# Optimization experiments

Hardware: AMD Instinct MI355X
Metric: run time of the kernel (lower is better)

Reference implementation:

```python
import jax, jax.numpy as jnp
import numpy as np

WINDOWS = [7, 15, 31, 63, 127]
MAX_W = max(WINDOWS)
PAD = MAX_W // 2 + 1  # 64, matches K.spatial_2d_padding amount
HALF = MAX_W // 2     # 63


def _sat(a):
    """Integral image (summed-area table) of zero-padded input, per original layer."""
    ap = jnp.pad(a, ((0, 0), (PAD, PAD), (PAD, PAD), (0, 0)))
    return jnp.cumsum(jnp.cumsum(ap, axis=1), axis=2)


def _multi_window_means(a):
    """Box means for all window sizes. a: [B,H,W,C] -> [B,n_wins,H,W,C].
    Computes the count SAT once (original redundantly recomputes it per window;
    math is identical)."""
    B, H, W, C = a.shape
    ii = _sat(a)
    cnt_ii = _sat(jnp.ones_like(a[:1, ..., :1]))  # [1, H+2P, W+2P, 1]

    def box(ii_, h, w):
        top = HALF - h // 2
        left = HALF - w // 2
        bot, right = top + h, left + w
        return (ii_[:, top:top + H, left:left + W]
                + ii_[:, bot:bot + H, right:right + W]
                - ii_[:, top:top + H, right:right + W]
                - ii_[:, bot:bot + H, left:left + W])

    means = [box(ii, h, h) / box(cnt_ii, h, h) for h in WINDOWS]
    return jnp.stack(means, axis=1)  # [B, n_wins, H, W, C]


def setup_inputs() -> dict:
    key = jax.random.key(0)
    k1, _ = jax.random.split(key)
    B, H, W, C = 8, 1024, 1024, 1
    n_wins = len(WINDOWS)
    x = jax.random.uniform(k1, (B, H, W, C), dtype=jnp.float32)  # normalized image in (0,1)
    k = jnp.full((1, n_wins, 1, 1, 1), 0.2, dtype=jnp.float32)   # init_k
    R = jnp.full((1, n_wins, 1, 1, 1), 0.5, dtype=jnp.float32)   # init_R
    return {"x": x, "k": k, "R": R}


def reference(x, k, R):
    E_x = _multi_window_means(x)          # [B,5,H,W,C]
    E_x2 = _multi_window_means(x * x)
    dev_x = jnp.sqrt(jnp.maximum(E_x2 - E_x * E_x, 1e-6))
    T = E_x * (1.0 + k * (dev_x / R - 1.0))
    return T.astype(jnp.float32)
```

## Files before the change

### kernel.cpp

```cpp
#include <hip/hip_runtime.h>
#include <cstddef>

#define B_ 8
#define H_ 1024
#define W_ 1024
#define NW_ 5
#define CHUNKS_ 8
#define CHROWS_ (H_ / CHUNKS_)

__global__ __launch_bounds__(256) void k_rowscan(const float* __restrict__ x,
                                                 float* __restrict__ P1,
                                                 float* __restrict__ P2) {
  const int y = blockIdx.x, b = blockIdx.y, tid = threadIdx.x;
  const size_t rowoff = ((size_t)b * H_ + y) * W_;
  const float4 v = reinterpret_cast<const float4*>(x + rowoff)[tid];

  float c1[4], c2[4];
  c1[0] = v.x - 0.5f; c1[1] = v.y - 0.5f; c1[2] = v.z - 0.5f; c1[3] = v.w - 0.5f;
  c2[0] = v.x * v.x - (1.0f / 3.0f);
  c2[1] = v.y * v.y - (1.0f / 3.0f);
  c2[2] = v.z * v.z - (1.0f / 3.0f);
  c2[3] = v.w * v.w - (1.0f / 3.0f);

  float i1[4], i2[4];
  i1[0] = c1[0]; i2[0] = c2[0];
  #pragma unroll
  for (int j = 1; j < 4; ++j) { i1[j] = i1[j - 1] + c1[j]; i2[j] = i2[j - 1] + c2[j]; }
  const float s1 = i1[3], s2 = i2[3];

  __shared__ float sh1[256], sh2[256];
  sh1[tid] = s1; sh2[tid] = s2;
  __syncthreads();
  #pragma unroll
  for (int off = 1; off < 256; off <<= 1) {
    float t1 = 0.f, t2 = 0.f;
    if (tid >= off) { t1 = sh1[tid - off]; t2 = sh2[tid - off]; }
    __syncthreads();
    sh1[tid] += t1; sh2[tid] += t2;
    __syncthreads();
  }
  const float e1 = sh1[tid] - s1;
  const float e2 = sh2[tid] - s2;

  float4 o1, o2;
  o1.x = e1 + i1[0]; o1.y = e1 + i1[1]; o1.z = e1 + i1[2]; o1.w = e1 + i1[3];
  o2.x = e2 + i2[0]; o2.y = e2 + i2[1]; o2.z = e2 + i2[2]; o2.w = e2 + i2[3];
  reinterpret_cast<float4*>(P1 + rowoff)[tid] = o1;
  reinterpret_cast<float4*>(P2 + rowoff)[tid] = o2;
}

__global__ __launch_bounds__(256) void k_colpart(const float* __restrict__ P1,
                                                 const float* __restrict__ P2,
                                                 float* __restrict__ part1,
                                                 float* __restrict__ part2) {
  const int x = blockIdx.x * 256 + threadIdx.x;
  const int ch = blockIdx.y, b = blockIdx.z;
  const float* p1 = P1 + ((size_t)b * H_ + (size_t)ch * CHROWS_) * W_ + x;
  const float* p2 = P2 + ((size_t)b * H_ + (size_t)ch * CHROWS_) * W_ + x;
  float s1 = 0.f, s2 = 0.f;
  #pragma unroll 8
  for (int i = 0; i < CHROWS_; ++i) {
    s1 += p1[(size_t)i * W_];
    s2 += p2[(size_t)i * W_];
  }
  const size_t o = ((size_t)(b * CHUNKS_ + ch)) * W_ + x;
  part1[o] = s1; part2[o] = s2;
}

__global__ __launch_bounds__(256) void k_chunkscan(float* __restrict__ part1,
                                                   float* __restrict__ part2) {
  const int idx = blockIdx.x * 256 + threadIdx.x;
  const int b = idx / W_, x = idx - b * W_;
  float r1 = 0.f, r2 = 0.f;
  #pragma unroll
  for (int ch = 0; ch < CHUNKS_; ++ch) {
    const size_t o = ((size_t)(b * CHUNKS_ + ch)) * W_ + x;
    const float v1 = part1[o], v2 = part2[o];
    part1[o] = r1; part2[o] = r2;
    r1 += v1; r2 += v2;
  }
}

__global__ __launch_bounds__(256) void k_colscan(float* __restrict__ P1,
                                                 float* __restrict__ P2,
                                                 const float* __restrict__ part1,
                                                 const float* __restrict__ part2) {
  const int x = blockIdx.x * 256 + threadIdx.x;
  const int ch = blockIdx.y, b = blockIdx.z;
  const size_t po = ((size_t)(b * CHUNKS_ + ch)) * W_ + x;
  float r1 = part1[po], r2 = part2[po];
  float* p1 = P1 + ((size_t)b * H_ + (size_t)ch * CHROWS_) * W_ + x;
  float* p2 = P2 + ((size_t)b * H_ + (size_t)ch * CHROWS_) * W_ + x;
  #pragma unroll 4
  for (int i = 0; i < CHROWS_; ++i) {
    const size_t o = (size_t)i * W_;
    r1 += p1[o]; p1[o] = r1;
    r2 += p2[o]; p2[o] = r2;
  }
}

__global__ __launch_bounds__(256) void k_out(const float* __restrict__ S1,
                                             const float* __restrict__ S2,
                                             const float* __restrict__ kk,
                                             const float* __restrict__ RR,
                                             float* __restrict__ out) {
  const int i = blockIdx.x;
  const int xcd = i & 7;
  const int s = i >> 3;
  const int b = s >> 7;
  const int y = xcd * 128 + (s & 127);
  const int t = threadIdx.x;

  __shared__ float lds[2 * NW_ * W_];

  const float* base1 = S1 + (size_t)b * H_ * W_;
  const float* base2 = S2 + (size_t)b * H_ * W_;
  const int rad[NW_] = {3, 7, 15, 31, 63};

  #pragma unroll
  for (int w = 0; w < NW_; ++w) {
    const int r = rad[w];
    const int yB = min(y + r, H_ - 1);
    const int yT = y - r - 1;
    const float4 fb1 = reinterpret_cast<const float4*>(base1 + (size_t)yB * W_)[t];
    const float4 fb2 = reinterpret_cast<const float4*>(base2 + (size_t)yB * W_)[t];
    float4 ft1 = {0.f, 0.f, 0.f, 0.f}, ft2 = {0.f, 0.f, 0.f, 0.f};
    if (yT >= 0) {
      ft1 = reinterpret_cast<const float4*>(base1 + (size_t)yT * W_)[t];
      ft2 = reinterpret_cast<const float4*>(base2 + (size_t)yT * W_)[t];
    }
    float4 d1, d2;
    d1.x = fb1.x - ft1.x; d1.y = fb1.y - ft1.y; d1.z = fb1.z - ft1.z; d1.w = fb1.w - ft1.w;
    d2.x = fb2.x - ft2.x; d2.y = fb2.y - ft2.y; d2.z = fb2.z - ft2.z; d2.w = fb2.w - ft2.w;
    reinterpret_cast<float4*>(lds + (size_t)(2 * w) * W_)[t] = d1;
    reinterpret_cast<float4*>(lds + (size_t)(2 * w + 1) * W_)[t] = d2;
  }
  __syncthreads();

  #pragma unroll
  for (int w = 0; w < NW_; ++w) {
    const int r = rad[w];
    const float kw = kk[w];
    const float invR = __builtin_amdgcn_rcpf(RR[w]);
    const int yB = min(y + r, H_ - 1);
    const float rows = (float)(yB - max(y - r, 0) + 1);
    const float* D1 = lds + (size_t)(2 * w) * W_;
    const float* D2 = lds + (size_t)(2 * w + 1) * W_;
    float* orow = out + (((size_t)(b * NW_ + w)) * H_ + y) * W_;
    #pragma unroll
    for (int kp = 0; kp < 4; ++kp) {
      const int xx = t + kp * 256;
      const int xR = min(xx + r, W_ - 1);
      const int xL = xx - r - 1;
      float s1 = D1[xR];
      float s2 = D2[xR];
      if (xL >= 0) { s1 -= D1[xL]; s2 -= D2[xL]; }
      const float cols = (float)(xR - max(xx - r, 0) + 1);
      const float inv = __builtin_amdgcn_rcpf(rows * cols);
      const float Ex  = s1 * inv + 0.5f;
      const float Ex2 = s2 * inv + (1.0f / 3.0f);
      const float var = Ex2 - Ex * Ex;
      const float dev = __builtin_amdgcn_sqrtf(fmaxf(var, 1e-6f));
      orow[xx] = Ex * (1.0f + kw * (dev * invR - 1.0f));
    }
  }
}

extern "C" void kernel_launch(void* const* d_in, const int* in_sizes, int n_in,
                              void* d_out, int out_size, void* d_ws, size_t ws_size,
                              hipStream_t stream) {
  const float* x  = (const float*)d_in[0];
  const float* kk = (const float*)d_in[1];
  const float* RR = (const float*)d_in[2];
  float* out = (float*)d_out;

  const size_t plane = (size_t)B_ * H_ * W_;
  float* P1 = (float*)d_ws;
  float* P2 = P1 + plane;
  float* part1 = P2 + plane;
  float* part2 = part1 + (size_t)B_ * CHUNKS_ * W_;

  k_rowscan <<<dim3(H_, B_),              256, 0, stream>>>(x, P1, P2);
  k_colpart <<<dim3(W_/256, CHUNKS_, B_), 256, 0, stream>>>(P1, P2, part1, part2);
  k_chunkscan<<<dim3((B_ * W_) / 256),    256, 0, stream>>>(part1, part2);
  k_colscan <<<dim3(W_/256, CHUNKS_, B_), 256, 0, stream>>>(P1, P2, part1, part2);
  k_out     <<<dim3(B_ * H_),             256, 0, stream>>>(P1, P2, kk, RR, out);
}
```

Measured before the change: 262.5 us.

## Fuse row scan with column chunk partial sums and drop chunk-scan kernel

The row prefix-scan kernel now also accumulates per-chunk column sums in registers and reduces them through LDS, so the separate column-partial pass that re-read P1/P2 is gone. Each wave scans whole rows with wave shuffles instead of block-wide LDS scans with barriers. The chunk-scan kernel is removed; k_colscan instead sums the preceding chunk partials itself. Chunks go from 8 to 32 to raise column-scan parallelism, but the row kernel then launches only 256 blocks, each walking 32 rows serially, which may underfill the GPU.

```diff
diff --git a/kernel.cpp b/kernel.cpp
--- a/kernel.cpp
+++ b/kernel.cpp
@@ -5,93 +5,99 @@
 #define H_ 1024
 #define W_ 1024
 #define NW_ 5
-#define CHUNKS_ 8
+#define CHUNKS_ 32
 #define CHROWS_ (H_ / CHUNKS_)
 
-__global__ __launch_bounds__(256) void k_rowscan(const float* __restrict__ x,
+__global__ __launch_bounds__(256) void k_rowpart(const float* __restrict__ x,
                                                  float* __restrict__ P1,
-                                                 float* __restrict__ P2) {
-  const int y = blockIdx.x, b = blockIdx.y, tid = threadIdx.x;
-  const size_t rowoff = ((size_t)b * H_ + y) * W_;
-  const float4 v = reinterpret_cast<const float4*>(x + rowoff)[tid];
-
-  float c1[4], c2[4];
-  c1[0] = v.x - 0.5f; c1[1] = v.y - 0.5f; c1[2] = v.z - 0.5f; c1[3] = v.w - 0.5f;
-  c2[0] = v.x * v.x - (1.0f / 3.0f);
-  c2[1] = v.y * v.y - (1.0f / 3.0f);
-  c2[2] = v.z * v.z - (1.0f / 3.0f);
-  c2[3] = v.w * v.w - (1.0f / 3.0f);
-
-  float i1[4], i2[4];
-  i1[0] = c1[0]; i2[0] = c2[0];
-  #pragma unroll
-  for (int j = 1; j < 4; ++j) { i1[j] = i1[j - 1] + c1[j]; i2[j] = i2[j - 1] + c2[j]; }
-  const float s1 = i1[3], s2 = i2[3];
-
-  __shared__ float sh1[256], sh2[256];
-  sh1[tid] = s1; sh2[tid] = s2;
-  __syncthreads();
-  #pragma unroll
-  for (int off = 1; off < 256; off <<= 1) {
-    float t1 = 0.f, t2 = 0.f;
-    if (tid >= off) { t1 = sh1[tid - off]; t2 = sh2[tid - off]; }
-    __syncthreads();
-    sh1[tid] += t1; sh2[tid] += t2;
-    __syncthreads();
-  }
-  const float e1 = sh1[tid] - s1;
-  const float e2 = sh2[tid] - s2;
-
-  float4 o1, o2;
-  o1.x = e1 + i1[0]; o1.y = e1 + i1[1]; o1.z = e1 + i1[2]; o1.w = e1 + i1[3];
-  o2.x = e2 + i2[0]; o2.y = e2 + i2[1]; o2.z = e2 + i2[2]; o2.w = e2 + i2[3];
-  reinterpret_cast<float4*>(P1 + rowoff)[tid] = o1;
-  reinterpret_cast<float4*>(P2 + rowoff)[tid] = o2;
-}
-
-__global__ __launch_bounds__(256) void k_colpart(const float* __restrict__ P1,
-                                                 const float* __restrict__ P2,
+                                                 float* __restrict__ P2,
                                                  float* __restrict__ part1,
                                                  float* __restrict__ part2) {
-  const int x = blockIdx.x * 256 + threadIdx.x;
-  const int ch = blockIdx.y, b = blockIdx.z;
-  const float* p1 = P1 + ((size_t)b * H_ + (size_t)ch * CHROWS_) * W_ + x;
-  const float* p2 = P2 + ((size_t)b * H_ + (size_t)ch * CHROWS_) * W_ + x;
-  float s1 = 0.f, s2 = 0.f;
-  #pragma unroll 8
-  for (int i = 0; i < CHROWS_; ++i) {
-    s1 += p1[(size_t)i * W_];
-    s2 += p2[(size_t)i * W_];
+  const int ch = blockIdx.x, b = blockIdx.y;
+  const int wave = threadIdx.x >> 6, lane = threadIdx.x & 63;
+  const int row0 = ch * CHROWS_ + wave * (CHROWS_ / 4);
+
+  float4 acc1[4], acc2[4];
+  #pragma unroll
+  for (int c = 0; c < 4; ++c) {
+    acc1[c] = make_float4(0.f, 0.f, 0.f, 0.f);
+    acc2[c] = make_float4(0.f, 0.f, 0.f, 0.f);
   }
-  const size_t o = ((size_t)(b * CHUNKS_ + ch)) * W_ + x;
-  part1[o] = s1; part2[o] = s2;
-}
 
-__global__ __launch_bounds__(256) void k_chunkscan(float* __restrict__ part1,
-                                                   float* __restrict__ part2) {
-  const int idx = blockIdx.x * 256 + threadIdx.x;
-  const int b = idx / W_, x = idx - b * W_;
-  float r1 = 0.f, r2 = 0.f;
+  for (int rr = 0; rr < CHROWS_ / 4; ++rr) {
+    const int y = row0 + rr;
+    const size_t rowoff = ((size_t)b * H_ + y) * W_;
+    float carry1 = 0.f, carry2 = 0.f;
+    #pragma unroll
+    for (int c = 0; c < 4; ++c) {
+      const float4 v = reinterpret_cast<const float4*>(x + rowoff + c * 256)[lane];
+      float l1[4], l2[4];
+      l1[0] = v.x - 0.5f;
+      l1[1] = l1[0] + (v.y - 0.5f);
+      l1[2] = l1[1] + (v.z - 0.5f);
+      l1[3] = l1[2] + (v.w - 0.5f);
+      l2[0] = v.x * v.x - (1.0f / 3.0f);
+      l2[1] = l2[0] + (v.y * v.y - (1.0f / 3.0f));
+      l2[2] = l2[1] + (v.z * v.z - (1.0f / 3.0f));
+      l2[3] = l2[2] + (v.w * v.w - (1.0f / 3.0f));
+      const float s1 = l1[3], s2 = l2[3];
+      float inc1 = s1, inc2 = s2;
+      #pragma unroll
+      for (int off = 1; off < 64; off <<= 1) {
+        const float t1 = __shfl_up(inc1, off);
+        const float t2 = __shfl_up(inc2, off);
+        if (lane >= off) { inc1 += t1; inc2 += t2; }
+      }
+      const float base1 = carry1 + inc1 - s1;
+      const float base2 = carry2 + inc2 - s2;
+      float4 o1, o2;
+      o1.x = base1 + l1[0]; o1.y = base1 + l1[1]; o1.z = base1 + l1[2]; o1.w = base1 + l1[3];
+      o2.x = base2 + l2[0]; o2.y = base2 + l2[1]; o2.z = base2 + l2[2]; o2.w = base2 + l2[3];
+      reinterpret_cast<float4*>(P1 + rowoff + c * 256)[lane] = o1;
+      reinterpret_cast<float4*>(P2 + rowoff + c * 256)[lane] = o2;
+      acc1[c].x += o1.x; acc1[c].y += o1.y; acc1[c].z += o1.z; acc1[c].w += o1.w;
+      acc2[c].x += o2.x; acc2[c].y += o2.y; acc2[c].z += o2.z; acc2[c].w += o2.w;
+      carry1 += __shfl(inc1, 63);
+      carry2 += __shfl(inc2, 63);
+    }
+  }
+
+  __shared__ float red[4][2][W_];
   #pragma unroll
-  for (int ch = 0; ch < CHUNKS_; ++ch) {
-    const size_t o = ((size_t)(b * CHUNKS_ + ch)) * W_ + x;
-    const float v1 = part1[o], v2 = part2[o];
-    part1[o] = r1; part2[o] = r2;
-    r1 += v1; r2 += v2;
+  for (int c = 0; c < 4; ++c) {
+    reinterpret_cast<float4*>(&red[wave][0][c * 256])[lane] = acc1[c];
+    reinterpret_cast<float4*>(&red[wave][1][c * 256])[lane] = acc2[c];
   }
+  __syncthreads();
+  const int t = threadIdx.x;
+  float4 r1 = make_float4(0.f, 0.f, 0.f, 0.f), r2 = r1;
+  #pragma unroll
+  for (int w = 0; w < 4; ++w) {
+    const float4 a = reinterpret_cast<const float4*>(&red[w][0][0])[t];
+    const float4 c2 = reinterpret_cast<const float4*>(&red[w][1][0])[t];
+    r1.x += a.x; r1.y += a.y; r1.z += a.z; r1.w += a.w;
+    r2.x += c2.x; r2.y += c2.y; r2.z += c2.z; r2.w += c2.w;
+  }
+  const size_t po = ((size_t)(b * CHUNKS_ + ch)) * W_;
+  reinterpret_cast<float4*>(part1 + po)[t] = r1;
+  reinterpret_cast<float4*>(part2 + po)[t] = r2;
 }
 
 __global__ __launch_bounds__(256) void k_colscan(float* __restrict__ P1,
                                                  float* __restrict__ P2,
                                                  const float* __restrict__ part1,
                                                  const float* __restrict__ part2) {
-  const int x = blockIdx.x * 256 + threadIdx.x;
+  const int xx = blockIdx.x * 256 + threadIdx.x;
   const int ch = blockIdx.y, b = blockIdx.z;
-  const size_t po = ((size_t)(b * CHUNKS_ + ch)) * W_ + x;
-  float r1 = part1[po], r2 = part2[po];
-  float* p1 = P1 + ((size_t)b * H_ + (size_t)ch * CHROWS_) * W_ + x;
-  float* p2 = P2 + ((size_t)b * H_ + (size_t)ch * CHROWS_) * W_ + x;
-  #pragma unroll 4
+  float r1 = 0.f, r2 = 0.f;
+  for (int c = 0; c < ch; ++c) {
+    const size_t o = ((size_t)(b * CHUNKS_ + c)) * W_ + xx;
+    r1 += part1[o];
+    r2 += part2[o];
+  }
+  float* p1 = P1 + ((size_t)b * H_ + (size_t)ch * CHROWS_) * W_ + xx;
+  float* p2 = P2 + ((size_t)b * H_ + (size_t)ch * CHROWS_) * W_ + xx;
+  #pragma unroll 8
   for (int i = 0; i < CHROWS_; ++i) {
     const size_t o = (size_t)i * W_;
     r1 += p1[o]; p1[o] = r1;
@@ -180,9 +186,7 @@
   float* part1 = P2 + plane;
   float* part2 = part1 + (size_t)B_ * CHUNKS_ * W_;
 
-  k_rowscan <<<dim3(H_, B_),              256, 0, stream>>>(x, P1, P2);
-  k_colpart <<<dim3(W_/256, CHUNKS_, B_), 256, 0, stream>>>(P1, P2, part1, part2);
-  k_chunkscan<<<dim3((B_ * W_) / 256),    256, 0, stream>>>(part1, part2);
-  k_colscan <<<dim3(W_/256, CHUNKS_, B_), 256, 0, stream>>>(P1, P2, part1, part2);
-  k_out     <<<dim3(B_ * H_),             256, 0, stream>>>(P1, P2, kk, RR, out);
+  k_rowpart <<<dim3(CHUNKS_, B_),          256, 0, stream>>>(x, P1, P2, part1, part2);
+  k_colscan <<<dim3(W_/256, CHUNKS_, B_),  256, 0, stream>>>(P1, P2, part1, part2);
+  k_out     <<<dim3(B_ * H_),              256, 0, stream>>>(P1, P2, kk, RR, out);
 }
```

Measured after the change: 251.7 us. -4.1%, faster.

## Replace row-scan pass with per-row LDS prefix scan inside output kernel

Applied to the files above, without the earlier changes.

Drops the separate row-scan kernel so the global workspace holds only column prefix sums, built directly from x. The output kernel takes row differences of those column sums and then runs a wave-level shuffle prefix scan in LDS for each of the ten rows before the box lookups. Column chunks grow from 8 to 32, and the chunk-offset scan is folded into the column-scan kernel, which now sums the earlier partials itself. This removes a full read and write of both planes and two launches, at the cost of extra scan work and a barrier in every output block.

```diff
diff --git a/kernel.cpp b/kernel.cpp
--- a/kernel.cpp
+++ b/kernel.cpp
@@ -5,102 +5,54 @@
 #define H_ 1024
 #define W_ 1024
 #define NW_ 5
-#define CHUNKS_ 8
-#define CHROWS_ (H_ / CHUNKS_)
+#define CH_ 32
+#define CHR_ (H_ / CH_)
 
-__global__ __launch_bounds__(256) void k_rowscan(const float* __restrict__ x,
-                                                 float* __restrict__ P1,
-                                                 float* __restrict__ P2) {
-  const int y = blockIdx.x, b = blockIdx.y, tid = threadIdx.x;
-  const size_t rowoff = ((size_t)b * H_ + y) * W_;
-  const float4 v = reinterpret_cast<const float4*>(x + rowoff)[tid];
 
-  float c1[4], c2[4];
-  c1[0] = v.x - 0.5f; c1[1] = v.y - 0.5f; c1[2] = v.z - 0.5f; c1[3] = v.w - 0.5f;
-  c2[0] = v.x * v.x - (1.0f / 3.0f);
-  c2[1] = v.y * v.y - (1.0f / 3.0f);
-  c2[2] = v.z * v.z - (1.0f / 3.0f);
-  c2[3] = v.w * v.w - (1.0f / 3.0f);
-
-  float i1[4], i2[4];
-  i1[0] = c1[0]; i2[0] = c2[0];
-  #pragma unroll
-  for (int j = 1; j < 4; ++j) { i1[j] = i1[j - 1] + c1[j]; i2[j] = i2[j - 1] + c2[j]; }
-  const float s1 = i1[3], s2 = i2[3];
-
-  __shared__ float sh1[256], sh2[256];
-  sh1[tid] = s1; sh2[tid] = s2;
-  __syncthreads();
-  #pragma unroll
-  for (int off = 1; off < 256; off <<= 1) {
-    float t1 = 0.f, t2 = 0.f;
-    if (tid >= off) { t1 = sh1[tid - off]; t2 = sh2[tid - off]; }
-    __syncthreads();
-    sh1[tid] += t1; sh2[tid] += t2;
-    __syncthreads();
-  }
-  const float e1 = sh1[tid] - s1;
-  const float e2 = sh2[tid] - s2;
-
-  float4 o1, o2;
-  o1.x = e1 + i1[0]; o1.y = e1 + i1[1]; o1.z = e1 + i1[2]; o1.w = e1 + i1[3];
-  o2.x = e2 + i2[0]; o2.y = e2 + i2[1]; o2.z = e2 + i2[2]; o2.w = e2 + i2[3];
-  reinterpret_cast<float4*>(P1 + rowoff)[tid] = o1;
-  reinterpret_cast<float4*>(P2 + rowoff)[tid] = o2;
-}
-
-__global__ __launch_bounds__(256) void k_colpart(const float* __restrict__ P1,
-                                                 const float* __restrict__ P2,
+__global__ __launch_bounds__(256) void k_colpart(const float* __restrict__ x,
                                                  float* __restrict__ part1,
                                                  float* __restrict__ part2) {
-  const int x = blockIdx.x * 256 + threadIdx.x;
+  const int xx = blockIdx.x * 256 + threadIdx.x;
   const int ch = blockIdx.y, b = blockIdx.z;
-  const float* p1 = P1 + ((size_t)b * H_ + (size_t)ch * CHROWS_) * W_ + x;
-  const float* p2 = P2 + ((size_t)b * H_ + (size_t)ch * CHROWS_) * W_ + x;
+  const float* p = x + ((size_t)b * H_ + (size_t)ch * CHR_) * W_ + xx;
   float s1 = 0.f, s2 = 0.f;
   #pragma unroll 8
-  for (int i = 0; i < CHROWS_; ++i) {
-    s1 += p1[(size_t)i * W_];
-    s2 += p2[(size_t)i * W_];
+  for (int i = 0; i < CHR_; ++i) {
+    const float v = p[(size_t)i * W_];
+    s1 += v - 0.5f;
+    s2 += v * v - (1.0f / 3.0f);
   }
-  const size_t o = ((size_t)(b * CHUNKS_ + ch)) * W_ + x;
+  const size_t o = ((size_t)(b * CH_ + ch)) * W_ + xx;
   part1[o] = s1; part2[o] = s2;
 }
 
-__global__ __launch_bounds__(256) void k_chunkscan(float* __restrict__ part1,
-                                                   float* __restrict__ part2) {
-  const int idx = blockIdx.x * 256 + threadIdx.x;
-  const int b = idx / W_, x = idx - b * W_;
+__global__ __launch_bounds__(256) void k_colscan(const float* __restrict__ x,
+                                                 float* __restrict__ C1,
+                                                 float* __restrict__ C2,
+                                                 const float* __restrict__ part1,
+                                                 const float* __restrict__ part2) {
+  const int xx = blockIdx.x * 256 + threadIdx.x;
+  const int ch = blockIdx.y, b = blockIdx.z;
   float r1 = 0.f, r2 = 0.f;
-  #pragma unroll
-  for (int ch = 0; ch < CHUNKS_; ++ch) {
-    const size_t o = ((size_t)(b * CHUNKS_ + ch)) * W_ + x;
-    const float v1 = part1[o], v2 = part2[o];
-    part1[o] = r1; part2[o] = r2;
-    r1 += v1; r2 += v2;
+  for (int c = 0; c < ch; ++c) {
+    const size_t o = ((size_t)(b * CH_ + c)) * W_ + xx;
+    r1 += part1[o];
+    r2 += part2[o];
+  }
+  const size_t base = ((size_t)b * H_ + (size_t)ch * CHR_) * W_ + xx;
+  #pragma unroll 8
+  for (int i = 0; i < CHR_; ++i) {
+    const size_t o = base + (size_t)i * W_;
+    const float v = x[o];
+    r1 += v - 0.5f;
+    r2 += v * v - (1.0f / 3.0f);
+    C1[o] = r1;
+    C2[o] = r2;
   }
 }
 
-__global__ __launch_bounds__(256) void k_colscan(float* __restrict__ P1,
-                                                 float* __restrict__ P2,
-                                                 const float* __restrict__ part1,
-                                                 const float* __restrict__ part2) {
-  const int x = blockIdx.x * 256 + threadIdx.x;
-  const int ch = blockIdx.y, b = blockIdx.z;
-  const size_t po = ((size_t)(b * CHUNKS_ + ch)) * W_ + x;
-  float r1 = part1[po], r2 = part2[po];
-  float* p1 = P1 + ((size_t)b * H_ + (size_t)ch * CHROWS_) * W_ + x;
-  float* p2 = P2 + ((size_t)b * H_ + (size_t)ch * CHROWS_) * W_ + x;
-  #pragma unroll 4
-  for (int i = 0; i < CHROWS_; ++i) {
-    const size_t o = (size_t)i * W_;
-    r1 += p1[o]; p1[o] = r1;
-    r2 += p2[o]; p2[o] = r2;
-  }
-}
-
-__global__ __launch_bounds__(256) void k_out(const float* __restrict__ S1,
-                                             const float* __restrict__ S2,
+__global__ __launch_bounds__(256) void k_out(const float* __restrict__ C1,
+                                             const float* __restrict__ C2,
                                              const float* __restrict__ kk,
                                              const float* __restrict__ RR,
                                              float* __restrict__ out) {
@@ -113,8 +65,8 @@
 
   __shared__ float lds[2 * NW_ * W_];
 
-  const float* base1 = S1 + (size_t)b * H_ * W_;
-  const float* base2 = S2 + (size_t)b * H_ * W_;
+  const float* base1 = C1 + (size_t)b * H_ * W_;
+  const float* base2 = C2 + (size_t)b * H_ * W_;
   const int rad[NW_] = {3, 7, 15, 31, 63};
 
   #pragma unroll
@@ -137,6 +89,32 @@
   }
   __syncthreads();
 
+  const int wave = t >> 6, lane = t & 63;
+  for (int p = wave; p < 2 * NW_; p += 4) {
+    float* D = lds + (size_t)p * W_;
+    float carry = 0.f;
+    #pragma unroll
+    for (int g = 0; g < 4; ++g) {
+      const float4 v = reinterpret_cast<const float4*>(D + g * 256)[lane];
+      const float l0 = v.x;
+      const float l1 = l0 + v.y;
+      const float l2 = l1 + v.z;
+      const float l3 = l2 + v.w;
+      float inc = l3;
+      #pragma unroll
+      for (int off = 1; off < 64; off <<= 1) {
+        const float u = __shfl_up(inc, off);
+        if (lane >= off) inc += u;
+      }
+      const float bse = carry + inc - l3;
+      float4 o;
+      o.x = bse + l0; o.y = bse + l1; o.z = bse + l2; o.w = bse + l3;
+      reinterpret_cast<float4*>(D + g * 256)[lane] = o;
+      carry += __shfl(inc, 63);
+    }
+  }
+  __syncthreads();
+
   #pragma unroll
   for (int w = 0; w < NW_; ++w) {
     const int r = rad[w];
@@ -144,17 +122,17 @@
     const float invR = __builtin_amdgcn_rcpf(RR[w]);
     const int yB = min(y + r, H_ - 1);
     const float rows = (float)(yB - max(y - r, 0) + 1);
-    const float* D1 = lds + (size_t)(2 * w) * W_;
-    const float* D2 = lds + (size_t)(2 * w + 1) * W_;
+    const float* H1 = lds + (size_t)(2 * w) * W_;
+    const float* H2 = lds + (size_t)(2 * w + 1) * W_;
     float* orow = out + (((size_t)(b * NW_ + w)) * H_ + y) * W_;
     #pragma unroll
     for (int kp = 0; kp < 4; ++kp) {
       const int xx = t + kp * 256;
       const int xR = min(xx + r, W_ - 1);
       const int xL = xx - r - 1;
-      float s1 = D1[xR];
-      float s2 = D2[xR];
-      if (xL >= 0) { s1 -= D1[xL]; s2 -= D2[xL]; }
+      float s1 = H1[xR];
+      float s2 = H2[xR];
+      if (xL >= 0) { s1 -= H1[xL]; s2 -= H2[xL]; }
       const float cols = (float)(xR - max(xx - r, 0) + 1);
       const float inv = __builtin_amdgcn_rcpf(rows * cols);
       const float Ex  = s1 * inv + 0.5f;
@@ -175,14 +153,12 @@
   float* out = (float*)d_out;
 
   const size_t plane = (size_t)B_ * H_ * W_;
-  float* P1 = (float*)d_ws;
-  float* P2 = P1 + plane;
-  float* part1 = P2 + plane;
-  float* part2 = part1 + (size_t)B_ * CHUNKS_ * W_;
+  float* C1 = (float*)d_ws;
+  float* C2 = C1 + plane;
+  float* part1 = C2 + plane;
+  float* part2 = part1 + (size_t)B_ * CH_ * W_;
 
-  k_rowscan <<<dim3(H_, B_),              256, 0, stream>>>(x, P1, P2);
-  k_colpart <<<dim3(W_/256, CHUNKS_, B_), 256, 0, stream>>>(P1, P2, part1, part2);
-  k_chunkscan<<<dim3((B_ * W_) / 256),    256, 0, stream>>>(part1, part2);
-  k_colscan <<<dim3(W_/256, CHUNKS_, B_), 256, 0, stream>>>(P1, P2, part1, part2);
-  k_out     <<<dim3(B_ * H_),             256, 0, stream>>>(P1, P2, kk, RR, out);
+  k_colpart <<<dim3(W_/256, CH_, B_), 256, 0, stream>>>(x, part1, part2);
+  k_colscan <<<dim3(W_/256, CH_, B_), 256, 0, stream>>>(x, C1, C2, part1, part2);
+  k_out     <<<dim3(B_ * H_),         256, 0, stream>>>(C1, C2, kk, RR, out);
 }
```

Measured after the change: 256.6 us. 2.3% less time.
